# Optimization experiments

Measured on AMD Instinct MI355X. Metric: run time of the kernel, lower is better.

The kernel has to match this reference:

```python
import jax, jax.numpy as jnp
import numpy as np
from itertools import combinations

S = 7                       # number of species (H,C,N,O,S,F,Cl)
RCR, RCA = 5.2, 3.5         # radial / angular cutoffs (Angstrom)
ETA_R, ETA_A, ZETA = 19.7, 12.5, 14.1
SHF_R = jnp.asarray(0.8 + 0.275 * np.arange(16), jnp.float32)        # 16 radial shifts
SHF_A = jnp.asarray(0.8 + 0.3375 * np.arange(8), jnp.float32)        # 8 angular radial shifts
SHF_Z = jnp.asarray((np.arange(4) + 0.5) * np.pi / 4, jnp.float32)   # 4 angle shifts
NPAIR = S * (S + 1) // 2    # 28 unordered species pairs
_t = np.zeros((S, S), np.int32); _c = 0
for _a in range(S):
    for _b in range(_a, S):
        _t[_a, _b] = _t[_b, _a] = _c; _c += 1
TRIU = jnp.asarray(_t)
AEV_DIM = S * 16 + NPAIR * 32   # 1008
M, H1, H2, H3 = 8, 256, 192, 160  # ensemble size and MLP widths


def _fc(d, rc):
    # torchani cutoff_cosine, masked for safety beyond rc
    return jnp.where(d < rc, 0.5 * jnp.cos(jnp.pi * d / rc) + 0.5, 0.0)


def compute_aev(sp, coords, atom_index12, triplet_index):
    # sp:[N] int, coords:[N,3], atom_index12:[2,P] half neighbor list,
    # triplet_index:[3,T] = (center, neighbor_j, neighbor_k)
    N = sp.shape[0]
    i, j = atom_index12[0], atom_index12[1]
    dvec = coords[j] - coords[i]
    dist = jnp.sqrt((dvec * dvec).sum(-1))
    fc = _fc(dist, RCR)
    rterm = 0.25 * jnp.exp(-ETA_R * (dist[:, None] - SHF_R) ** 2) * fc[:, None]  # [P,16]
    rad = jnp.zeros((N * S, 16), rterm.dtype)
    rad = rad.at[i * S + sp[j]].add(rterm).at[j * S + sp[i]].add(rterm)
    rad = rad.reshape(N, S * 16)

    c, a, b = triplet_index[0], triplet_index[1], triplet_index[2]
    v1 = coords[a] - coords[c]
    v2 = coords[b] - coords[c]
    d1 = jnp.sqrt((v1 * v1).sum(-1))
    d2 = jnp.sqrt((v2 * v2).sum(-1))
    cosang = 0.95 * (v1 * v2).sum(-1) / (d1 * d2)   # 0.95 numerical-safety factor as in torchani
    ang = jnp.arccos(cosang)
    fcj = _fc(d1, RCA) * _fc(d2, RCA)
    f1 = ((1.0 + jnp.cos(ang[:, None] - SHF_Z)) / 2.0) ** ZETA              # [T,4]
    f2 = jnp.exp(-ETA_A * ((d1 + d2)[:, None] / 2.0 - SHF_A) ** 2)          # [T,8]
    aterm = 2.0 * (f2[:, :, None] * f1[:, None, :]).reshape(-1, 32) * fcj[:, None]  # [T,32]
    pidx = TRIU[sp[a], sp[b]]
    angv = jnp.zeros((N * NPAIR, 32), aterm.dtype).at[c * NPAIR + pidx].add(aterm)
    return jnp.concatenate([rad, angv.reshape(N, NPAIR * 32)], axis=-1)     # [N,1008]


def _energy_and_force(species, coordinates, atom_index12, triplet_index, sgp,
                      W1, b1, W2, b2, W3, b3, W4, b4, sae):
    sp = species[0]
    sgpv = sgp[0]

    def total(coords):
        aev = compute_aev(sp, coords[0], atom_index12, triplet_index)       # [N,1008]
        h = jax.nn.celu(jnp.einsum('na,msab->msnb', aev, W1) + b1[:, :, None, :], alpha=0.1)
        h = jax.nn.celu(jnp.einsum('msnb,msbc->msnc', h, W2) + b2[:, :, None, :], alpha=0.1)
        h = jax.nn.celu(jnp.einsum('msnc,mscd->msnd', h, W3) + b3[:, :, None, :], alpha=0.1)
        e = jnp.einsum('msnd,msd->msn', h, W4) + b4[:, :, None]             # [M,S,N]
        onehot = (sgpv[None, :] == jnp.arange(S)[:, None]).astype(e.dtype)  # ghosts (-1) -> all-zero
        atomic = (e * onehot[None]).sum(1).mean(0)                           # [N] ensemble mean
        atomic = atomic + jnp.where(sgpv >= 0, sae[jnp.clip(sgpv, 0)], 0.0)  # energy shifter SAEs
        return atomic.sum()

    E = total(coordinates)
    force = -jax.grad(total)(coordinates)   # autograd force as in forward_total
    return E[None], force


def setup_inputs() -> dict:
    key = jax.random.key(0)
    n = 14; N = n ** 3   # 2744 atoms on a jittered cubic lattice (2.5 A spacing)
    ar = np.arange(n)
    gx, gy, gz = np.meshgrid(ar, ar, ar, indexing='ij')
    pos = np.stack([gx, gy, gz], -1).reshape(-1, 3)
    lid = lambda p: (p[:, 0] * n + p[:, 1]) * n + p[:, 2]
    # half neighbor list: all lattice offsets with |r| <= 5.2/2.5 lattice units
    half = [(1,0,0),(0,1,0),(0,0,1),(1,1,0),(1,-1,0),(1,0,1),(1,0,-1),(0,1,1),(0,1,-1),
            (1,1,1),(1,1,-1),(1,-1,1),(1,-1,-1),(2,0,0),(0,2,0),(0,0,2)]
    ei, ej = [], []
    for off in half:
        q = pos + np.array(off)
        m = ((q >= 0) & (q < n)).all(1)
        ei.append(lid(pos[m])); ej.append(lid(q[m]))
    atom_index12 = np.stack([np.concatenate(ei), np.concatenate(ej)]).astype(np.int32)
    # angular triplets: pairs of unit-offset neighbors (within Rca=3.5 A) per center
    unit = [(1,0,0),(-1,0,0),(0,1,0),(0,-1,0),(0,0,1),(0,0,-1)]
    nb = np.full((N, 6), -1, np.int64)
    for t, off in enumerate(unit):
        q = pos + np.array(off)
        m = ((q >= 0) & (q < n)).all(1)
        nb[lid(pos[m]), t] = lid(q[m])
    tc, tj, tk = [], [], []
    for a_, b_ in combinations(range(6), 2):
        m = (nb[:, a_] >= 0) & (nb[:, b_] >= 0)
        tc.append(np.nonzero(m)[0]); tj.append(nb[m, a_]); tk.append(nb[m, b_])
    triplet_index = np.stack([np.concatenate(tc), np.concatenate(tj), np.concatenate(tk)]).astype(np.int32)
    rng = np.random.default_rng(0)
    species = rng.integers(0, S, (1, N)).astype(np.int32)
    nghost = 250
    sgp = species.copy(); sgp[0, N - nghost:] = -1   # ghost atoms padded with -1
    coords = (pos.astype(np.float32) * 2.5 + 0.15 * rng.standard_normal((N, 3)).astype(np.float32))[None]
    ks = jax.random.split(key, 9)
    D = AEV_DIM
    W1 = jax.random.normal(ks[0], (M, S, D, H1), jnp.float32) * (D ** -0.5)
    b1 = 0.01 * jax.random.normal(ks[1], (M, S, H1), jnp.float32)
    W2 = jax.random.normal(ks[2], (M, S, H1, H2), jnp.float32) * (H1 ** -0.5)
    b2 = 0.01 * jax.random.normal(ks[3], (M, S, H2), jnp.float32)
    W3 = jax.random.normal(ks[4], (M, S, H2, H3), jnp.float32) * (H2 ** -0.5)
    b3 = 0.01 * jax.random.normal(ks[5], (M, S, H3), jnp.float32)
    W4 = jax.random.normal(ks[6], (M, S, H3), jnp.float32) * (H3 ** -0.5)
    b4 = 0.01 * jax.random.normal(ks[7], (M, S), jnp.float32)
    sae = jax.random.normal(ks[8], (S,), jnp.float32)
    return {
        'species': jnp.asarray(species), 'coordinates': jnp.asarray(coords),
        'atom_index12': jnp.asarray(atom_index12), 'triplet_index': jnp.asarray(triplet_index),
        'species_ghost_as_padding': jnp.asarray(sgp),
        'W1': W1, 'b1': b1, 'W2': W2, 'b2': b2, 'W3': W3, 'b3': b3, 'W4': W4, 'b4': b4, 'sae': sae,
    }


def reference(species, coordinates, atom_index12, triplet_index, species_ghost_as_padding,
              W1, b1, W2, b2, W3, b3, W4, b4, sae):
    return _energy_and_force(species, coordinates, atom_index12, triplet_index,
                             species_ghost_as_padding, W1, b1, W2, b2, W3, b3, W4, b4, sae)
```

## Files before the change

kernel.cpp:

```cpp
#include <hip/hip_runtime.h>
#include <math.h>

constexpr int SPEC = 7;
constexpr int DAEV = 1008;
constexpr int RADN = 112;
constexpr int H1W = 256, H2W = 192, H3W = 160;
constexpr int MENS = 8;
constexpr float ALPHA = 0.1f;
constexpr float RCR_ = 5.2f, RCA_ = 3.5f;
constexpr float ETAR = 19.7f, ETAA = 12.5f, ZETA_ = 14.1f;
constexpr float PIF = 3.14159265358979323846f;

enum { MODE_FWD = 0, MODE_BWD = 1, MODE_PLAIN = 2 };

typedef _Float16 f16x8 __attribute__((ext_vector_type(8)));
typedef float f32x4 __attribute__((ext_vector_type(4)));

__device__ __forceinline__ f32x4 mfma16(f16x8 a, f16x8 b, f32x4 c) {
    return __builtin_amdgcn_mfma_f32_16x16x32_f16(a, b, c, 0, 0, 0);
}

__device__ __forceinline__ void cvt8(float4 u0, float4 u1, f16x8& h, f16x8& l) {
    float x[8] = {u0.x, u0.y, u0.z, u0.w, u1.x, u1.y, u1.z, u1.w};
    #pragma unroll
    for (int e = 0; e < 8; ++e) {
        _Float16 hh = (_Float16)x[e];
        h[e] = hh;
        l[e] = (_Float16)(x[e] - (float)hh);
    }
}

__global__ __launch_bounds__(256) void build_lists_k(
    const int* __restrict__ sgp, int* __restrict__ counts,
    int* __restrict__ lists, int N)
{
    int n = blockIdx.x * blockDim.x + threadIdx.x;
    if (n >= N) return;
    int g = sgp[n];
    if (g >= 0) {
        int p = atomicAdd(&counts[g], 1);
        lists[g * N + p] = n;
    }
}

__global__ __launch_bounds__(256) void radial_fwd_k(
    const int* __restrict__ ai12, const int* __restrict__ spec,
    const float* __restrict__ coord, float* __restrict__ aev, int P)
{
    int p = blockIdx.x * blockDim.x + threadIdx.x;
    if (p >= P) return;
    int i = ai12[p], j = ai12[P + p];
    float dx = coord[3 * j + 0] - coord[3 * i + 0];
    float dy = coord[3 * j + 1] - coord[3 * i + 1];
    float dz = coord[3 * j + 2] - coord[3 * i + 2];
    float d = sqrtf(dx * dx + dy * dy + dz * dz);
    float fc = (d < RCR_) ? (0.5f * cosf(PIF * d / RCR_) + 0.5f) : 0.f;
    int spi = spec[i], spj = spec[j];
    float* bi = aev + (size_t)i * DAEV + spj * 16;
    float* bj = aev + (size_t)j * DAEV + spi * 16;
    #pragma unroll
    for (int k = 0; k < 16; ++k) {
        float sh = 0.8f + 0.275f * k;
        float t = d - sh;
        float v = 0.25f * expf(-ETAR * t * t) * fc;
        atomicAdd(bi + k, v);
        atomicAdd(bj + k, v);
    }
}

__global__ __launch_bounds__(256) void angular_fwd_k(
    const int* __restrict__ tri, const int* __restrict__ spec,
    const float* __restrict__ coord, float* __restrict__ aev, int T)
{
    int t = blockIdx.x * blockDim.x + threadIdx.x;
    if (t >= T) return;
    int c = tri[t], a = tri[T + t], b = tri[2 * T + t];
    float cx = coord[3 * c], cy = coord[3 * c + 1], cz = coord[3 * c + 2];
    float v1x = coord[3 * a] - cx, v1y = coord[3 * a + 1] - cy, v1z = coord[3 * a + 2] - cz;
    float v2x = coord[3 * b] - cx, v2y = coord[3 * b + 1] - cy, v2z = coord[3 * b + 2] - cz;
    float d1 = sqrtf(v1x * v1x + v1y * v1y + v1z * v1z);
    float d2 = sqrtf(v2x * v2x + v2y * v2y + v2z * v2z);
    float u = v1x * v2x + v1y * v2y + v1z * v2z;
    float ca = 0.95f * u / (d1 * d2);
    float sa = sqrtf(fmaxf(1.f - ca * ca, 0.f));
    float fc1 = (d1 < RCA_) ? (0.5f * cosf(PIF * d1 / RCA_) + 0.5f) : 0.f;
    float fc2 = (d2 < RCA_) ? (0.5f * cosf(PIF * d2 / RCA_) + 0.5f) : 0.f;
    float fcj = fc1 * fc2;
    float savg = 0.5f * (d1 + d2);
    int s1 = spec[a], s2 = spec[b];
    int lo = min(s1, s2), hi = max(s1, s2);
    int pidx = lo * SPEC - (lo * (lo - 1)) / 2 + (hi - lo);
    float* ob = aev + (size_t)c * DAEV + RADN + pidx * 32;
    const float CZ[4] = {0.92387953f, 0.38268343f, -0.38268343f, -0.92387953f};
    const float SZ[4] = {0.38268343f, 0.92387953f, 0.92387953f, 0.38268343f};
    float f1[4];
    #pragma unroll
    for (int zz = 0; zz < 4; ++zz) {
        float cd = ca * CZ[zz] + sa * SZ[zz];
        float base = fmaxf(0.5f * (1.f + cd), 0.f);
        f1[zz] = powf(base, ZETA_);
    }
    #pragma unroll
    for (int q = 0; q < 8; ++q) {
        float sh = 0.8f + 0.3375f * q;
        float tq = savg - sh;
        float f2 = expf(-ETAA * tq * tq);
        float b2 = 2.f * f2 * fcj;
        #pragma unroll
        for (int zz = 0; zz < 4; ++zz)
            atomicAdd(ob + q * 4 + zz, b2 * f1[zz]);
    }
}

template<bool DO_O, bool DO_T>
__global__ __launch_bounds__(256) void wconv_k(
    const float* __restrict__ W,
    _Float16* __restrict__ oH, _Float16* __restrict__ oL,
    _Float16* __restrict__ tH, _Float16* __restrict__ tL,
    int K, int C, int ldt)
{
    __shared__ _Float16 sh[64][65];
    __shared__ _Float16 sl[64][65];
    const int z = blockIdx.z;
    const int k0 = blockIdx.y * 64, c0 = blockIdx.x * 64;
    const float* Wz = W + (size_t)z * K * C;
    const int c = threadIdx.x & 63, qr = threadIdx.x >> 6;
    #pragma unroll
    for (int rr = 0; rr < 16; ++rr) {
        int r = qr * 16 + rr;
        int k = k0 + r, cc = c0 + c;
        float v = (k < K && cc < C) ? Wz[(size_t)k * C + cc] : 0.f;
        _Float16 h = (_Float16)v;
        _Float16 l = (_Float16)(v - (float)h);
        if (DO_O && k < K && cc < C) {
            oH[(size_t)z * K * C + (size_t)k * C + cc] = h;
            oL[(size_t)z * K * C + (size_t)k * C + cc] = l;
        }
        if (DO_T) { sh[r][c] = h; sl[r][c] = l; }
    }
    if (DO_T) {
        __syncthreads();
        #pragma unroll
        for (int rr = 0; rr < 16; ++rr) {
            int r = qr * 16 + rr;
            int crow = c0 + r, kcol = k0 + c;
            if (crow < C && kcol < ldt) {
                tH[(size_t)z * C * ldt + (size_t)crow * ldt + kcol] = sh[c][r];
                tL[(size_t)z * C * ldt + (size_t)crow * ldt + kcol] = sl[c][r];
            }
        }
    }
}

template<int MODE, int ASRC, int BSRC, bool MCONCAT>
__global__ __launch_bounds__(256) void mgemm_k(
    const void* __restrict__ Ah_, const void* __restrict__ Al_,
    const void* __restrict__ Bh_, const void* __restrict__ Bl_,
    const float* __restrict__ bias, float* __restrict__ cF,
    _Float16* __restrict__ cH, _Float16* __restrict__ cL,
    const int* __restrict__ lists, const int* __restrict__ counts,
    int N, int K, int KA, int H, int lda, int ldb, int ldc,
    size_t aStrM, size_t bStrZ, size_t cStrM)
{
    __shared__ f16x8 AhS[4][64];
    __shared__ f16x8 AlS[4][64];
    __shared__ float4 BU4[1056];
    __shared__ int atomsS[64];

    f16x8* BhS = (f16x8*)BU4;
    f16x8* BlS = BhS + 512;
    float* Bf = (float*)BU4;

    const int z = blockIdx.z;
    int m, sp_;
    if (MCONCAT) { sp_ = z; m = 0; } else { m = z / SPEC; sp_ = z - m * SPEC; }
    const int cnt = counts[sp_];
    const int row0 = blockIdx.y * 64;
    if (row0 >= cnt) return;
    const int col0 = blockIdx.x * 128;
    const int tid = threadIdx.x;
    const int w = tid >> 6, lane = tid & 63;

    const int rA = min(row0 + lane, cnt - 1);
    const int atomA = lists[sp_ * N + rA];
    if (tid < 64) atomsS[tid] = atomA;

    const int bc0 = min(col0 + lane, H - 1);
    const int bc1 = min(col0 + 64 + lane, H - 1);

    f16x8 rAh, rAl;
    float4 rAf0, rAf1;
    f16x8 rBh0, rBl0, rBh1, rBl1;
    float4 rBf[4];

    auto LOAD = [&](int k0s) {
        int kk = k0s + w * 8;
        if constexpr (ASRC == 0) {
            const _Float16* ah = (const _Float16*)Ah_;
            const _Float16* al = (const _Float16*)Al_;
            size_t ao;
            if constexpr (MCONCAT) {
                int mm = kk >> 8, kr = kk & 255;
                ao = ((size_t)mm * N + atomA) * (size_t)lda + kr;
            } else {
                ao = (size_t)m * aStrM + (size_t)atomA * lda + kk;
            }
            rAh = *(const f16x8*)(ah + ao);
            rAl = *(const f16x8*)(al + ao);
        } else {
            const float* af = (const float*)Ah_;
            if (kk < KA) {
                const float* p = af + (size_t)atomA * lda + kk;
                rAf0 = *(const float4*)p;
                rAf1 = *(const float4*)(p + 4);
            } else {
                rAf0 = make_float4(0.f, 0.f, 0.f, 0.f);
                rAf1 = rAf0;
            }
        }
        if constexpr (BSRC == 0) {
            const _Float16* bh = (const _Float16*)Bh_;
            const _Float16* bl = (const _Float16*)Bl_;
            size_t b0 = (size_t)z * bStrZ + (size_t)bc0 * ldb + kk;
            size_t b1 = (size_t)z * bStrZ + (size_t)bc1 * ldb + kk;
            rBh0 = *(const f16x8*)(bh + b0);
            rBh1 = *(const f16x8*)(bh + b1);
            rBl0 = *(const f16x8*)(bl + b0);
            rBl1 = *(const f16x8*)(bl + b1);
        } else if constexpr (BSRC == 1) {
            const float* bf = (const float*)Bh_;
            int mm = kk >> 8, kr = kk & 255;
            size_t b0 = ((size_t)(mm * SPEC + sp_) * DAEV + bc0) * (size_t)ldb + kr;
            size_t b1 = ((size_t)(mm * SPEC + sp_) * DAEV + bc1) * (size_t)ldb + kr;
            rBf[0] = *(const float4*)(bf + b0);
            rBf[1] = *(const float4*)(bf + b0 + 4);
            rBf[2] = *(const float4*)(bf + b1);
            rBf[3] = *(const float4*)(bf + b1 + 4);
        } else {
            const float* bf = (const float*)Bh_ + (size_t)z * bStrZ;
            #pragma unroll
            for (int p = 0; p < 4; ++p) {
                int kl = p * 8 + (tid >> 5);
                int kg = k0s + kl;
                if (kg < KA)
                    rBf[p] = *(const float4*)(bf + (size_t)kg * ldb + col0 + (tid & 31) * 4);
                else
                    rBf[p] = make_float4(0.f, 0.f, 0.f, 0.f);
            }
        }
    };

    auto WRITE = [&]() {
        if constexpr (ASRC == 0) {
            AhS[w][lane] = rAh;
            AlS[w][lane] = rAl;
        } else {
            f16x8 h, l;
            cvt8(rAf0, rAf1, h, l);
            AhS[w][lane] = h;
            AlS[w][lane] = l;
        }
        if constexpr (BSRC == 0) {
            BhS[w * 128 + lane] = rBh0;
            BhS[w * 128 + 64 + lane] = rBh1;
            BlS[w * 128 + lane] = rBl0;
            BlS[w * 128 + 64 + lane] = rBl1;
        } else if constexpr (BSRC == 1) {
            f16x8 h, l;
            cvt8(rBf[0], rBf[1], h, l);
            BhS[w * 128 + lane] = h;
            BlS[w * 128 + lane] = l;
            cvt8(rBf[2], rBf[3], h, l);
            BhS[w * 128 + 64 + lane] = h;
            BlS[w * 128 + 64 + lane] = l;
        } else {
            #pragma unroll
            for (int p = 0; p < 4; ++p) {
                int kl = p * 8 + (tid >> 5);
                *(float4*)(Bf + kl * 132 + (tid & 31) * 4) = rBf[p];
            }
        }
    };

    const int wr = w >> 1, wc = w & 1;
    const int fr = lane & 15, q = lane >> 4;

    f32x4 acc[2][4];
    #pragma unroll
    for (int mi = 0; mi < 2; ++mi)
        #pragma unroll
        for (int ni = 0; ni < 4; ++ni)
            acc[mi][ni] = (f32x4){0.f, 0.f, 0.f, 0.f};

    const int nt = K / 32;
    LOAD(0);

    for (int t = 0; t < nt; ++t) {
        __syncthreads();
        WRITE();
        __syncthreads();
        if (t + 1 < nt) LOAD((t + 1) * 32);

        f16x8 fah[2], fal[2], fbh[4], fbl[4];
        #pragma unroll
        for (int mi = 0; mi < 2; ++mi) {
            int r = wr * 32 + mi * 16 + fr;
            fah[mi] = AhS[q][r];
            fal[mi] = AlS[q][r];
        }
        if constexpr (BSRC <= 1) {
            #pragma unroll
            for (int ni = 0; ni < 4; ++ni) {
                int c = wc * 64 + ni * 16 + fr;
                fbh[ni] = BhS[q * 128 + c];
                fbl[ni] = BlS[q * 128 + c];
            }
        } else {
            #pragma unroll
            for (int ni = 0; ni < 4; ++ni) {
                int c = wc * 64 + ni * 16 + fr;
                #pragma unroll
                for (int j = 0; j < 8; ++j) {
                    float v = Bf[(q * 8 + j) * 132 + c];
                    _Float16 hh = (_Float16)v;
                    fbh[ni][j] = hh;
                    fbl[ni][j] = (_Float16)(v - (float)hh);
                }
            }
        }
        #pragma unroll
        for (int mi = 0; mi < 2; ++mi)
            #pragma unroll
            for (int ni = 0; ni < 4; ++ni) {
                acc[mi][ni] = mfma16(fah[mi], fbl[ni], acc[mi][ni]);
                acc[mi][ni] = mfma16(fal[mi], fbh[ni], acc[mi][ni]);
                acc[mi][ni] = mfma16(fah[mi], fbh[ni], acc[mi][ni]);
            }
    }

    const float* brow = (MODE == MODE_FWD) ? (bias + (size_t)z * H) : nullptr;
    #pragma unroll
    for (int mi = 0; mi < 2; ++mi) {
        #pragma unroll
        for (int r = 0; r < 4; ++r) {
            int rl = wr * 32 + mi * 16 + q * 4 + r;
            if (row0 + rl >= cnt) continue;
            int atom = atomsS[rl];
            size_t rowoff = (size_t)m * cStrM + (size_t)atom * ldc;
            #pragma unroll
            for (int ni = 0; ni < 4; ++ni) {
                int col = col0 + wc * 64 + ni * 16 + fr;
                if (col >= H) continue;
                float v = acc[mi][ni][r];
                size_t idx = rowoff + col;
                if (MODE == MODE_FWD) {
                    v += brow[col];
                    v = (v > 0.f) ? v : ALPHA * expm1f(v * (1.f / ALPHA));
                    _Float16 hh = (_Float16)v;
                    cH[idx] = hh;
                    cL[idx] = (_Float16)(v - (float)hh);
                } else if (MODE == MODE_BWD) {
                    float hprev = (float)cH[idx] + (float)cL[idx];
                    float D = (hprev > 0.f) ? 1.f : (hprev * (1.f / ALPHA) + 1.f);
                    v *= D;
                    _Float16 hh = (_Float16)v;
                    cH[idx] = hh;
                    cL[idx] = (_Float16)(v - (float)hh);
                } else {
                    cF[idx] = v;
                }
            }
        }
    }
}

__global__ __launch_bounds__(256) void l4_k(
    _Float16* __restrict__ h3H, _Float16* __restrict__ h3L,
    const float* __restrict__ W4, const float* __restrict__ b4,
    const int* __restrict__ lists, const int* __restrict__ counts,
    float* __restrict__ Eout, int N)
{
    const int z = blockIdx.y;
    const int m = z / SPEC, s = z - m * SPEC;
    const int cnt = counts[s];
    const int sub = threadIdx.x >> 3;
    const int l8 = threadIdx.x & 7;
    const int row = blockIdx.x * 32 + sub;

    __shared__ float bsum;
    if (threadIdx.x == 0) bsum = 0.f;
    __syncthreads();

    if (row < cnt) {
        int atom = lists[s * N + row];
        size_t base = ((size_t)m * N + atom) * H3W;
        const float* w4 = W4 + (size_t)z * H3W;
        float sum = 0.f;
        for (int k = l8; k < H3W; k += 8) {
            float h = (float)h3H[base + k] + (float)h3L[base + k];
            float wv = w4[k];
            sum += h * wv;
            float D = (h > 0.f) ? 1.f : (h * 10.f + 1.f);
            float g = 0.125f * wv * D;
            _Float16 gh = (_Float16)g;
            h3H[base + k] = gh;
            h3L[base + k] = (_Float16)(g - (float)gh);
        }
        sum += __shfl_xor(sum, 1);
        sum += __shfl_xor(sum, 2);
        sum += __shfl_xor(sum, 4);
        if (l8 == 0) atomicAdd(&bsum, sum + b4[z]);
    }
    __syncthreads();
    if (threadIdx.x == 0) atomicAdd(Eout, 0.125f * bsum);
}

__global__ __launch_bounds__(256) void radial_bwd_k(
    const int* __restrict__ ai12, const int* __restrict__ spec,
    const float* __restrict__ coord, const float* __restrict__ daev,
    float* __restrict__ grad, int P)
{
    int p = blockIdx.x * blockDim.x + threadIdx.x;
    if (p >= P) return;
    int i = ai12[p], j = ai12[P + p];
    float dx = coord[3 * j + 0] - coord[3 * i + 0];
    float dy = coord[3 * j + 1] - coord[3 * i + 1];
    float dz = coord[3 * j + 2] - coord[3 * i + 2];
    float d = sqrtf(dx * dx + dy * dy + dz * dz);
    float fc, dfc;
    if (d < RCR_) {
        float ph = PIF * d / RCR_;
        fc = 0.5f * cosf(ph) + 0.5f;
        dfc = -0.5f * sinf(ph) * (PIF / RCR_);
    } else { fc = 0.f; dfc = 0.f; }
    int spi = spec[i], spj = spec[j];
    const float* gi = daev + (size_t)i * DAEV + spj * 16;
    const float* gj = daev + (size_t)j * DAEV + spi * 16;
    float gs = 0.f;
    #pragma unroll
    for (int k = 0; k < 16; ++k) {
        float sh = 0.8f + 0.275f * k;
        float t = d - sh;
        float ex = expf(-ETAR * t * t);
        float g = gi[k] + gj[k];
        gs += g * 0.25f * ex * (dfc - 2.f * ETAR * t * fc);
    }
    float invd = 1.f / d;
    float gx = gs * dx * invd, gy = gs * dy * invd, gz = gs * dz * invd;
    atomicAdd(&grad[3 * j + 0], gx);  atomicAdd(&grad[3 * j + 1], gy);  atomicAdd(&grad[3 * j + 2], gz);
    atomicAdd(&grad[3 * i + 0], -gx); atomicAdd(&grad[3 * i + 1], -gy); atomicAdd(&grad[3 * i + 2], -gz);
}

__global__ __launch_bounds__(256) void angular_bwd_k(
    const int* __restrict__ tri, const int* __restrict__ spec,
    const float* __restrict__ coord, const float* __restrict__ daev,
    float* __restrict__ grad, int T)
{
    int t = blockIdx.x * blockDim.x + threadIdx.x;
    if (t >= T) return;
    int c = tri[t], a = tri[T + t], b = tri[2 * T + t];
    float cx = coord[3 * c], cy = coord[3 * c + 1], cz = coord[3 * c + 2];
    float v1x = coord[3 * a] - cx, v1y = coord[3 * a + 1] - cy, v1z = coord[3 * a + 2] - cz;
    float v2x = coord[3 * b] - cx, v2y = coord[3 * b + 1] - cy, v2z = coord[3 * b + 2] - cz;
    float d1 = sqrtf(v1x * v1x + v1y * v1y + v1z * v1z);
    float d2 = sqrtf(v2x * v2x + v2y * v2y + v2z * v2z);
    float u = v1x * v2x + v1y * v2y + v1z * v2z;
    float inv12 = 1.f / (d1 * d2);
    float ca = 0.95f * u * inv12;
    float sa = sqrtf(fmaxf(1.f - ca * ca, 1e-12f));
    float fc1, dfc1, fc2, dfc2;
    if (d1 < RCA_) {
        float ph = PIF * d1 / RCA_;
        fc1 = 0.5f * cosf(ph) + 0.5f;
        dfc1 = -0.5f * sinf(ph) * (PIF / RCA_);
    } else { fc1 = 0.f; dfc1 = 0.f; }
    if (d2 < RCA_) {
        float ph = PIF * d2 / RCA_;
        fc2 = 0.5f * cosf(ph) + 0.5f;
        dfc2 = -0.5f * sinf(ph) * (PIF / RCA_);
    } else { fc2 = 0.f; dfc2 = 0.f; }
    float fcj = fc1 * fc2;
    float savg = 0.5f * (d1 + d2);
    int s1 = spec[a], s2 = spec[b];
    int lo = min(s1, s2), hi = max(s1, s2);
    int pidx = lo * SPEC - (lo * (lo - 1)) / 2 + (hi - lo);
    const float* gb = daev + (size_t)c * DAEV + RADN + pidx * 32;
    const float CZ[4] = {0.92387953f, 0.38268343f, -0.38268343f, -0.92387953f};
    const float SZ[4] = {0.38268343f, 0.92387953f, 0.92387953f, 0.38268343f};
    float f1[4], df1[4];
    #pragma unroll
    for (int zz = 0; zz < 4; ++zz) {
        float cd = ca * CZ[zz] + sa * SZ[zz];
        float sd = sa * CZ[zz] - ca * SZ[zz];
        float base = fmaxf(0.5f * (1.f + cd), 0.f);
        float pm1 = powf(base, ZETA_ - 1.f);
        f1[zz] = pm1 * base;
        df1[zz] = ZETA_ * pm1 * (-0.5f * sd);
    }
    float A_ = 0.f, B_ = 0.f, Cc = 0.f;
    #pragma unroll
    for (int q = 0; q < 8; ++q) {
        float sh = 0.8f + 0.3375f * q;
        float tq = savg - sh;
        float f2 = expf(-ETAA * tq * tq);
        float df2 = -ETAA * tq * f2;
        #pragma unroll
        for (int zz = 0; zz < 4; ++zz) {
            float G2 = 2.f * gb[q * 4 + zz];
            A_ += G2 * f2 * df1[zz];
            B_ += G2 * df2 * f1[zz];
            Cc += G2 * f2 * f1[zz];
        }
    }
    A_ *= fcj; B_ *= fcj;
    float C1 = Cc * dfc1 * fc2;
    float C2 = Cc * fc1 * dfc2;
    float cA = -A_ / sa;
    float k12 = cA * 0.95f * inv12;
    float coef1 = (cA * (-ca) / d1 + B_ + C1) / d1;
    float coef2 = (cA * (-ca) / d2 + B_ + C2) / d2;
    float g1x = coef1 * v1x + k12 * v2x;
    float g1y = coef1 * v1y + k12 * v2y;
    float g1z = coef1 * v1z + k12 * v2z;
    float g2x = coef2 * v2x + k12 * v1x;
    float g2y = coef2 * v2y + k12 * v1y;
    float g2z = coef2 * v2z + k12 * v1z;
    atomicAdd(&grad[3 * a + 0], g1x); atomicAdd(&grad[3 * a + 1], g1y); atomicAdd(&grad[3 * a + 2], g1z);
    atomicAdd(&grad[3 * b + 0], g2x); atomicAdd(&grad[3 * b + 1], g2y); atomicAdd(&grad[3 * b + 2], g2z);
    atomicAdd(&grad[3 * c + 0], -(g1x + g2x));
    atomicAdd(&grad[3 * c + 1], -(g1y + g2y));
    atomicAdd(&grad[3 * c + 2], -(g1z + g2z));
}

__global__ __launch_bounds__(256) void finalize_k(
    const float* __restrict__ grad, const int* __restrict__ sgp,
    const float* __restrict__ sae, float* __restrict__ out, int N)
{
    int n = blockIdx.x * blockDim.x + threadIdx.x;
    __shared__ float bs;
    if (threadIdx.x == 0) bs = 0.f;
    __syncthreads();
    float v = 0.f;
    if (n < N) {
        out[1 + 3 * n + 0] = -grad[3 * n + 0];
        out[1 + 3 * n + 1] = -grad[3 * n + 1];
        out[1 + 3 * n + 2] = -grad[3 * n + 2];
        int g = sgp[n];
        if (g >= 0) v = sae[g];
    }
    atomicAdd(&bs, v);
    __syncthreads();
    if (threadIdx.x == 0) atomicAdd(out, bs);
}

extern "C" void kernel_launch(void* const* d_in, const int* in_sizes, int n_in,
                              void* d_out, int out_size, void* d_ws, size_t ws_size,
                              hipStream_t stream)
{
    (void)n_in; (void)out_size; (void)ws_size;
    const int* species = (const int*)d_in[0];
    const float* coords = (const float*)d_in[1];
    const int* ai12 = (const int*)d_in[2];
    const int* tri = (const int*)d_in[3];
    const int* sgp = (const int*)d_in[4];
    const float* W1 = (const float*)d_in[5];
    const float* b1 = (const float*)d_in[6];
    const float* W2 = (const float*)d_in[7];
    const float* b2 = (const float*)d_in[8];
    const float* W3 = (const float*)d_in[9];
    const float* b3 = (const float*)d_in[10];
    const float* W4 = (const float*)d_in[11];
    const float* b4 = (const float*)d_in[12];
    const float* sae = (const float*)d_in[13];
    float* out = (float*)d_out;

    const int N = in_sizes[0];
    const int P = in_sizes[2] / 2;
    const int T = in_sizes[3] / 3;
    const size_t NM = (size_t)MENS * N;

    float* ws = (float*)d_ws;
    size_t off = 0;
    auto alloc = [&](size_t nf) { float* p = ws + off; off += nf; return p; };

    float* aev = alloc((size_t)N * DAEV);
    _Float16* H1h = (_Float16*)alloc(NM * 128);
    _Float16* H1l = (_Float16*)alloc(NM * 128);
    _Float16* H2h = (_Float16*)alloc(NM * 96);
    _Float16* H2l = (_Float16*)alloc(NM * 96);
    _Float16* H3h = (_Float16*)alloc(NM * 80);
    _Float16* H3l = (_Float16*)alloc(NM * 80);
    _Float16* Wh = (_Float16*)alloc((size_t)56 * 96 * 256);
    _Float16* Wl = (_Float16*)alloc((size_t)56 * 96 * 256);
    float* grad = alloc((size_t)N * 3);
    int* counts = (int*)alloc(8);
    int* lists = (int*)alloc((size_t)SPEC * N);
    float* daev = aev;

    hipMemsetAsync(aev, 0, (size_t)N * DAEV * sizeof(float), stream);
    hipMemsetAsync(grad, 0, (size_t)N * 3 * sizeof(float), stream);
    hipMemsetAsync(counts, 0, 8 * sizeof(int), stream);
    hipMemsetAsync(d_out, 0, sizeof(float), stream);

    build_lists_k<<<(N + 255) / 256, 256, 0, stream>>>(sgp, counts, lists, N);
    radial_fwd_k<<<(P + 255) / 256, 256, 0, stream>>>(ai12, species, coords, aev, P);
    angular_fwd_k<<<(T + 255) / 256, 256, 0, stream>>>(tri, species, coords, aev, T);

    const int rt = (N + 63) / 64;

    mgemm_k<MODE_FWD, 1, 2, false><<<dim3(2, rt, 56), 256, 0, stream>>>(
        aev, nullptr, W1, nullptr, b1, nullptr, H1h, H1l,
        lists, counts, N, 1024, 1008, 256, 1008, 256, 256,
        0, (size_t)1008 * 256, (size_t)N * 256);

    wconv_k<false, true><<<dim3(3, 4, 56), 256, 0, stream>>>(
        W2, nullptr, nullptr, Wh, Wl, 256, 192, 256);
    mgemm_k<MODE_FWD, 0, 0, false><<<dim3(2, rt, 56), 256, 0, stream>>>(
        H1h, H1l, Wh, Wl, b2, nullptr, H2h, H2l,
        lists, counts, N, 256, 256, 192, 256, 256, 192,
        (size_t)N * 256, (size_t)192 * 256, (size_t)N * 192);

    wconv_k<false, true><<<dim3(3, 3, 56), 256, 0, stream>>>(
        W3, nullptr, nullptr, Wh, Wl, 192, 160, 192);
    mgemm_k<MODE_FWD, 0, 0, false><<<dim3(2, rt, 56), 256, 0, stream>>>(
        H2h, H2l, Wh, Wl, b3, nullptr, H3h, H3l,
        lists, counts, N, 192, 192, 160, 192, 192, 160,
        (size_t)N * 192, (size_t)160 * 192, (size_t)N * 160);

    l4_k<<<dim3((N + 31) / 32, 56), 256, 0, stream>>>(
        H3h, H3l, W4, b4, lists, counts, out, N);

    hipMemsetAsync(daev, 0, (size_t)N * DAEV * sizeof(float), stream);

    wconv_k<true, false><<<dim3(3, 3, 56), 256, 0, stream>>>(
        W3, Wh, Wl, nullptr, nullptr, 192, 160, 0);
    mgemm_k<MODE_BWD, 0, 0, false><<<dim3(2, rt, 56), 256, 0, stream>>>(
        H3h, H3l, Wh, Wl, nullptr, nullptr, H2h, H2l,
        lists, counts, N, 160, 160, 192, 160, 160, 192,
        (size_t)N * 160, (size_t)192 * 160, (size_t)N * 192);

    wconv_k<true, false><<<dim3(3, 4, 56), 256, 0, stream>>>(
        W2, Wh, Wl, nullptr, nullptr, 256, 192, 0);
    mgemm_k<MODE_BWD, 0, 0, false><<<dim3(2, rt, 56), 256, 0, stream>>>(
        H2h, H2l, Wh, Wl, nullptr, nullptr, H1h, H1l,
        lists, counts, N, 192, 192, 256, 192, 192, 256,
        (size_t)N * 192, (size_t)256 * 192, (size_t)N * 256);

    mgemm_k<MODE_PLAIN, 0, 1, true><<<dim3(8, rt, 7), 256, 0, stream>>>(
        H1h, H1l, W1, nullptr, nullptr, daev, nullptr, nullptr,
        lists, counts, N, 2048, 2048, 1008, 256, 256, 1008,
        0, 0, 0);

    radial_bwd_k<<<(P + 255) / 256, 256, 0, stream>>>(ai12, species, coords, daev, grad, P);
    angular_bwd_k<<<(T + 255) / 256, 256, 0, stream>>>(tri, species, coords, daev, grad, T);
    finalize_k<<<(N + 255) / 256, 256, 0, stream>>>(grad, sgp, sae, out, N);
}
```

Before: 862.7 us.

## Split-K the dAEV backward GEMM with atomics and pre-convert W1 tiles once

The final MCONCAT GEMM, which produces the AEV gradient, is split along K into four chunks. This gives four times as many blocks in z, and the partial sums are accumulated into the zeroed daev buffer with atomicAdd. The forward layer-1 GEMM no longer stores fp32 W1 tiles in shared memory and splits them into fp16 hi/lo halves on every fragment read. Instead each thread loads per-column values and converts them once before writing the f16 shared tiles, which also shrinks shared memory. The trade-off is atomic traffic on daev, run-to-run nondeterministic summation order, and uncoalesced scalar W1 loads in place of float4 loads.

```diff
diff --git a/kernel.cpp b/kernel.cpp
--- a/kernel.cpp
+++ b/kernel.cpp
@@ -152,7 +152,7 @@
     }
 }
 
-template<int MODE, int ASRC, int BSRC, bool MCONCAT>
+template<int MODE, int ASRC, int BSRC, bool MCONCAT, int SPLITK>
 __global__ __launch_bounds__(256) void mgemm_k(
     const void* __restrict__ Ah_, const void* __restrict__ Al_,
     const void* __restrict__ Bh_, const void* __restrict__ Bl_,
@@ -164,16 +164,19 @@
 {
     __shared__ f16x8 AhS[4][64];
     __shared__ f16x8 AlS[4][64];
-    __shared__ float4 BU4[1056];
+    __shared__ f16x8 BhS[4][128];
+    __shared__ f16x8 BlS[4][128];
     __shared__ int atomsS[64];
 
-    f16x8* BhS = (f16x8*)BU4;
-    f16x8* BlS = BhS + 512;
-    float* Bf = (float*)BU4;
-
     const int z = blockIdx.z;
-    int m, sp_;
-    if (MCONCAT) { sp_ = z; m = 0; } else { m = z / SPEC; sp_ = z - m * SPEC; }
+    int m, sp_, chunk;
+    if (MCONCAT) {
+        sp_ = (SPLITK > 1) ? (z % SPEC) : z;
+        chunk = (SPLITK > 1) ? (z / SPEC) : 0;
+        m = 0;
+    } else {
+        m = z / SPEC; sp_ = z - m * SPEC; chunk = 0;
+    }
     const int cnt = counts[sp_];
     const int row0 = blockIdx.y * 64;
     if (row0 >= cnt) return;
@@ -191,7 +194,8 @@
     f16x8 rAh, rAl;
     float4 rAf0, rAf1;
     f16x8 rBh0, rBl0, rBh1, rBl1;
-    float4 rBf[4];
+    float4 rBq[4];
+    float rB0f[8], rB1f[8];
 
     auto LOAD = [&](int k0s) {
         int kk = k0s + w * 8;
@@ -232,20 +236,22 @@
             int mm = kk >> 8, kr = kk & 255;
             size_t b0 = ((size_t)(mm * SPEC + sp_) * DAEV + bc0) * (size_t)ldb + kr;
             size_t b1 = ((size_t)(mm * SPEC + sp_) * DAEV + bc1) * (size_t)ldb + kr;
-            rBf[0] = *(const float4*)(bf + b0);
-            rBf[1] = *(const float4*)(bf + b0 + 4);
-            rBf[2] = *(const float4*)(bf + b1);
-            rBf[3] = *(const float4*)(bf + b1 + 4);
+            rBq[0] = *(const float4*)(bf + b0);
+            rBq[1] = *(const float4*)(bf + b0 + 4);
+            rBq[2] = *(const float4*)(bf + b1);
+            rBq[3] = *(const float4*)(bf + b1 + 4);
         } else {
             const float* bf = (const float*)Bh_ + (size_t)z * bStrZ;
             #pragma unroll
-            for (int p = 0; p < 4; ++p) {
-                int kl = p * 8 + (tid >> 5);
-                int kg = k0s + kl;
-                if (kg < KA)
-                    rBf[p] = *(const float4*)(bf + (size_t)kg * ldb + col0 + (tid & 31) * 4);
-                else
-                    rBf[p] = make_float4(0.f, 0.f, 0.f, 0.f);
+            for (int j = 0; j < 8; ++j) {
+                int kg = kk + j;
+                float v0 = 0.f, v1 = 0.f;
+                if (kg < KA) {
+                    v0 = bf[(size_t)kg * ldb + bc0];
+                    v1 = bf[(size_t)kg * ldb + bc1];
+                }
+                rB0f[j] = v0;
+                rB1f[j] = v1;
             }
         }
     };
@@ -261,24 +267,31 @@
             AlS[w][lane] = l;
         }
         if constexpr (BSRC == 0) {
-            BhS[w * 128 + lane] = rBh0;
-            BhS[w * 128 + 64 + lane] = rBh1;
-            BlS[w * 128 + lane] = rBl0;
-            BlS[w * 128 + 64 + lane] = rBl1;
+            BhS[w][lane] = rBh0;
+            BhS[w][64 + lane] = rBh1;
+            BlS[w][lane] = rBl0;
+            BlS[w][64 + lane] = rBl1;
         } else if constexpr (BSRC == 1) {
             f16x8 h, l;
-            cvt8(rBf[0], rBf[1], h, l);
-            BhS[w * 128 + lane] = h;
-            BlS[w * 128 + lane] = l;
-            cvt8(rBf[2], rBf[3], h, l);
-            BhS[w * 128 + 64 + lane] = h;
-            BlS[w * 128 + 64 + lane] = l;
+            cvt8(rBq[0], rBq[1], h, l);
+            BhS[w][lane] = h;
+            BlS[w][lane] = l;
+            cvt8(rBq[2], rBq[3], h, l);
+            BhS[w][64 + lane] = h;
+            BlS[w][64 + lane] = l;
         } else {
+            f16x8 h0, l0, h1, l1;
             #pragma unroll
-            for (int p = 0; p < 4; ++p) {
-                int kl = p * 8 + (tid >> 5);
-                *(float4*)(Bf + kl * 132 + (tid & 31) * 4) = rBf[p];
+            for (int j = 0; j < 8; ++j) {
+                _Float16 ha = (_Float16)rB0f[j];
+                h0[j] = ha; l0[j] = (_Float16)(rB0f[j] - (float)ha);
+                _Float16 hb = (_Float16)rB1f[j];
+                h1[j] = hb; l1[j] = (_Float16)(rB1f[j] - (float)hb);
             }
+            BhS[w][lane] = h0;
+            BlS[w][lane] = l0;
+            BhS[w][64 + lane] = h1;
+            BlS[w][64 + lane] = l1;
         }
     };
 
@@ -292,14 +305,16 @@
         for (int ni = 0; ni < 4; ++ni)
             acc[mi][ni] = (f32x4){0.f, 0.f, 0.f, 0.f};
 
-    const int nt = K / 32;
-    LOAD(0);
+    const int KC = (SPLITK > 1) ? (K / SPLITK) : K;
+    const int kbeg = chunk * KC;
+    const int nt = KC / 32;
+    LOAD(kbeg);
 
     for (int t = 0; t < nt; ++t) {
         __syncthreads();
         WRITE();
         __syncthreads();
-        if (t + 1 < nt) LOAD((t + 1) * 32);
+        if (t + 1 < nt) LOAD(kbeg + (t + 1) * 32);
 
         f16x8 fah[2], fal[2], fbh[4], fbl[4];
         #pragma unroll
@@ -308,25 +323,11 @@
             fah[mi] = AhS[q][r];
             fal[mi] = AlS[q][r];
         }
-        if constexpr (BSRC <= 1) {
-            #pragma unroll
-            for (int ni = 0; ni < 4; ++ni) {
-                int c = wc * 64 + ni * 16 + fr;
-                fbh[ni] = BhS[q * 128 + c];
-                fbl[ni] = BlS[q * 128 + c];
-            }
-        } else {
-            #pragma unroll
-            for (int ni = 0; ni < 4; ++ni) {
-                int c = wc * 64 + ni * 16 + fr;
-                #pragma unroll
-                for (int j = 0; j < 8; ++j) {
-                    float v = Bf[(q * 8 + j) * 132 + c];
-                    _Float16 hh = (_Float16)v;
-                    fbh[ni][j] = hh;
-                    fbl[ni][j] = (_Float16)(v - (float)hh);
-                }
-            }
+        #pragma unroll
+        for (int ni = 0; ni < 4; ++ni) {
+            int c = wc * 64 + ni * 16 + fr;
+            fbh[ni] = BhS[q][c];
+            fbl[ni] = BlS[q][c];
         }
         #pragma unroll
         for (int mi = 0; mi < 2; ++mi)
@@ -367,7 +368,8 @@
                     cH[idx] = hh;
                     cL[idx] = (_Float16)(v - (float)hh);
                 } else {
-                    cF[idx] = v;
+                    if (SPLITK > 1) atomicAdd(cF + idx, v);
+                    else cF[idx] = v;
                 }
             }
         }
@@ -608,21 +610,21 @@
 
     const int rt = (N + 63) / 64;
 
-    mgemm_k<MODE_FWD, 1, 2, false><<<dim3(2, rt, 56), 256, 0, stream>>>(
+    mgemm_k<MODE_FWD, 1, 2, false, 1><<<dim3(2, rt, 56), 256, 0, stream>>>(
         aev, nullptr, W1, nullptr, b1, nullptr, H1h, H1l,
         lists, counts, N, 1024, 1008, 256, 1008, 256, 256,
         0, (size_t)1008 * 256, (size_t)N * 256);
 
     wconv_k<false, true><<<dim3(3, 4, 56), 256, 0, stream>>>(
         W2, nullptr, nullptr, Wh, Wl, 256, 192, 256);
-    mgemm_k<MODE_FWD, 0, 0, false><<<dim3(2, rt, 56), 256, 0, stream>>>(
+    mgemm_k<MODE_FWD, 0, 0, false, 1><<<dim3(2, rt, 56), 256, 0, stream>>>(
         H1h, H1l, Wh, Wl, b2, nullptr, H2h, H2l,
         lists, counts, N, 256, 256, 192, 256, 256, 192,
         (size_t)N * 256, (size_t)192 * 256, (size_t)N * 192);
 
     wconv_k<false, true><<<dim3(3, 3, 56), 256, 0, stream>>>(
         W3, nullptr, nullptr, Wh, Wl, 192, 160, 192);
-    mgemm_k<MODE_FWD, 0, 0, false><<<dim3(2, rt, 56), 256, 0, stream>>>(
+    mgemm_k<MODE_FWD, 0, 0, false, 1><<<dim3(2, rt, 56), 256, 0, stream>>>(
         H2h, H2l, Wh, Wl, b3, nullptr, H3h, H3l,
         lists, counts, N, 192, 192, 160, 192, 192, 160,
         (size_t)N * 192, (size_t)160 * 192, (size_t)N * 160);
@@ -634,19 +636,19 @@
 
     wconv_k<true, false><<<dim3(3, 3, 56), 256, 0, stream>>>(
         W3, Wh, Wl, nullptr, nullptr, 192, 160, 0);
-    mgemm_k<MODE_BWD, 0, 0, false><<<dim3(2, rt, 56), 256, 0, stream>>>(
+    mgemm_k<MODE_BWD, 0, 0, false, 1><<<dim3(2, rt, 56), 256, 0, stream>>>(
         H3h, H3l, Wh, Wl, nullptr, nullptr, H2h, H2l,
         lists, counts, N, 160, 160, 192, 160, 160, 192,
         (size_t)N * 160, (size_t)192 * 160, (size_t)N * 192);
 
     wconv_k<true, false><<<dim3(3, 4, 56), 256, 0, stream>>>(
         W2, Wh, Wl, nullptr, nullptr, 256, 192, 0);
-    mgemm_k<MODE_BWD, 0, 0, false><<<dim3(2, rt, 56), 256, 0, stream>>>(
+    mgemm_k<MODE_BWD, 0, 0, false, 1><<<dim3(2, rt, 56), 256, 0, stream>>>(
         H2h, H2l, Wh, Wl, nullptr, nullptr, H1h, H1l,
         lists, counts, N, 192, 192, 256, 192, 192, 256,
         (size_t)N * 192, (size_t)256 * 192, (size_t)N * 256);
 
-    mgemm_k<MODE_PLAIN, 0, 1, true><<<dim3(8, rt, 7), 256, 0, stream>>>(
+    mgemm_k<MODE_PLAIN, 0, 1, true, 4><<<dim3(8, rt, 28), 256, 0, stream>>>(
         H1h, H1l, W1, nullptr, nullptr, daev, nullptr, nullptr,
         lists, counts, N, 2048, 2048, 1008, 256, 256, 1008,
         0, 0, 0);
```

Measured after the change: 779.1 us. -9.7%, faster.
